# Performance work log

Hardware: AMD Instinct MI355X
Metric: run time of the kernel (lower is better)

Reference implementation:

```python
import jax, jax.numpy as jnp
import numpy as np

H = 768      # hidden_size
NH = 12      # num_heads
HD = H // NH # head_dim = 64


def setup_inputs() -> dict:
    key = jax.random.key(0)
    k1, k2, k3 = jax.random.split(key, 3)
    x = jax.random.normal(k1, (4, 2048, H), dtype=jnp.float32)
    # nn.Linear weights are [out, in]; we store transposed [in, out] for x @ W
    w_qkv = jax.random.normal(k2, (H, 3 * H), dtype=jnp.float32) * (1.0 / np.sqrt(H))
    w_out = jax.random.normal(k3, (H, H), dtype=jnp.float32) * (1.0 / np.sqrt(H))
    return {"x": x, "w_qkv": w_qkv, "w_out": w_out}


def reference(x, w_qkv, w_out):
    B, S, _ = x.shape
    qkv = (x @ w_qkv).reshape(B, S, 3, NH, HD)
    qkv = jnp.transpose(qkv, (2, 0, 3, 1, 4))  # [3, B, NH, S, HD]
    q, k, v = qkv[0], qkv[1], qkv[2]
    scale = 1.0 / np.sqrt(HD)
    scores = jnp.einsum('bhqd,bhkd->bhqk', q, k) * scale  # [B,NH,S,S]
    causal = jnp.tril(jnp.ones((S, S), dtype=bool))
    scores = jnp.where(causal, scores, jnp.finfo(scores.dtype).min)
    attn = jax.nn.softmax(scores, axis=-1)
    out = jnp.einsum('bhqk,bhkd->bhqd', attn, v)          # [B,NH,S,HD]
    out = jnp.transpose(out, (0, 2, 1, 3)).reshape(B, S, H)
    return out @ w_out
```

## Files before the change

kernel.cpp:

```cpp
#include <hip/hip_runtime.h>
#include <type_traits>

#define S_LEN 2048
#define HID   768
#define NHEAD 12
#define HDIM  64
#define BATCH 4

typedef __attribute__((ext_vector_type(4))) float float4v;
typedef __attribute__((ext_vector_type(8))) short short8;
typedef __attribute__((ext_vector_type(4))) short short4v;
typedef __attribute__((ext_vector_type(2))) int int2v;

__device__ __forceinline__ short f2b(float f) {
  unsigned u = __float_as_uint(f);
  u += 0x7fff + ((u >> 16) & 1);
  return (short)(u >> 16);
}

__device__ __forceinline__ unsigned pkbf(float a, float b) {
#if __has_builtin(__builtin_amdgcn_cvt_pk_bf16_f32)
  typedef __attribute__((ext_vector_type(2))) __bf16 bf2;
  bf2 r = __builtin_amdgcn_cvt_pk_bf16_f32(a, b);
  return *(unsigned*)&r;
#else
  return ((unsigned)(unsigned short)f2b(a)) |
         (((unsigned)(unsigned short)f2b(b)) << 16);
#endif
}

__device__ __forceinline__ float fexp2(float x) {
#if __has_builtin(__builtin_amdgcn_exp2f)
  return __builtin_amdgcn_exp2f(x);
#else
  return __expf(x * 0.69314718056f);
#endif
}

__device__ __forceinline__ void g2l16(const short* g, short* l) {
  __builtin_amdgcn_global_load_lds(
      (const __attribute__((address_space(1))) void*)g,
      (__attribute__((address_space(3))) void*)l, 16, 0, 0);
}

__global__ __launch_bounds__(256) void prepass(const float* __restrict__ x,
                                               const float* __restrict__ w_qkv,
                                               const float* __restrict__ w_out,
                                               short* __restrict__ xb,
                                               short* __restrict__ wqkvT,
                                               short* __restrict__ woutT) {
  __shared__ float tile[64][65];
  const int blk = blockIdx.x;
  if (blk < 3072) {
    int i = blk * 2048 + threadIdx.x * 8;
    float4v a = *(const float4v*)&x[i];
    float4v b = *(const float4v*)&x[i + 4];
    short8 o;
#pragma unroll
    for (int j = 0; j < 4; j++) { o[j] = f2b(a[j]); o[j + 4] = f2b(b[j]); }
    *(short8*)&xb[i] = o;
    return;
  }
  const float* W; short* WT; int N_, scaleN, idx;
  if (blk < 3504) { idx = blk - 3072; W = w_qkv; WT = wqkvT; N_ = 3 * HID; scaleN = HID; }
  else            { idx = blk - 3504; W = w_out; WT = woutT; N_ = HID;     scaleN = 0;  }
  const int nblk = N_ / 64;
  const int n0 = (idx % nblk) * 64, k0 = (idx / nblk) * 64;
  const int tx = threadIdx.x & 63, ty = threadIdx.x >> 6;
#pragma unroll
  for (int r = 0; r < 16; r++) {
    int row = r * 4 + ty;
    tile[row][tx] = W[(size_t)(k0 + row) * N_ + n0 + tx];
  }
  __syncthreads();
#pragma unroll
  for (int r = 0; r < 16; r++) {
    int row = r * 4 + ty;
    float sc = (n0 + row < scaleN) ? 0.18033688011f : 1.0f;
    WT[(size_t)(n0 + row) * HID + k0 + tx] = f2b(tile[tx][row] * sc);
  }
}

template <int OUT>
__global__ __launch_bounds__(256) void gemm_bt(const short* __restrict__ A,
                                               const short* __restrict__ Bt,
                                               float* __restrict__ Cf,
                                               short* __restrict__ Cq,
                                               short* __restrict__ vT,
                                               int M, int N, int K) {
  __shared__ __align__(16) short As[2][128 * 32];
  __shared__ __align__(16) short Bs[2][128 * 32];
  const int tid = threadIdx.x;
  const int w = tid >> 6, lane = tid & 63;
  const int quad = lane >> 4, lm = lane & 15;
  const int m0 = blockIdx.y * 128, n0 = blockIdx.x * 128;
  const int mo = (w & 1) * 64, no = (w >> 1) * 64;

  float4v acc[4][4];
#pragma unroll
  for (int i = 0; i < 4; i++)
#pragma unroll
    for (int j = 0; j < 4; j++) acc[i][j] = (float4v)0.0f;

  const int srow = w * 32 + (lane >> 2);
  const int scol = (lane & 3) * 8;
  const short* Ag = A + (size_t)(m0 + srow) * K + scol;
  const short* Bg = Bt + (size_t)(n0 + srow) * K + scol;

  for (int kb = 0; kb < K; kb += 64) {
#pragma unroll
    for (int s = 0; s < 2; s++) {
      short* Al = &As[s][(w * 32) * 32];
      short* Bl = &Bs[s][(w * 32) * 32];
      g2l16(Ag + kb + s * 32, Al);
      g2l16(Ag + kb + s * 32 + (size_t)16 * K, Al + 16 * 32);
      g2l16(Bg + kb + s * 32, Bl);
      g2l16(Bg + kb + s * 32 + (size_t)16 * K, Bl + 16 * 32);
    }
    __syncthreads();

#pragma unroll
    for (int s = 0; s < 2; s++) {
      short8 af[4], bf[4];
#pragma unroll
      for (int i = 0; i < 4; i++)
        af[i] = *(const short8*)&As[s][(mo + i * 16 + lm) * 32 + quad * 8];
#pragma unroll
      for (int j = 0; j < 4; j++)
        bf[j] = *(const short8*)&Bs[s][(no + j * 16 + lm) * 32 + quad * 8];
#pragma unroll
      for (int i = 0; i < 4; i++)
#pragma unroll
        for (int j = 0; j < 4; j++)
          acc[i][j] = __builtin_amdgcn_mfma_f32_16x16x32_bf16(af[i], bf[j], acc[i][j], 0, 0, 0);
    }
    __syncthreads();
  }

  if constexpr (OUT == 0) {
#pragma unroll
    for (int i = 0; i < 4; i++)
#pragma unroll
      for (int j = 0; j < 4; j++)
#pragma unroll
        for (int r = 0; r < 4; r++)
          Cf[(size_t)(m0 + mo + i * 16 + quad * 4 + r) * N + n0 + no + j * 16 + lm] =
              acc[i][j][r];
  } else {
    if (n0 >= 2 * HID) {
      const int b = m0 >> 11;
      const int s0 = (m0 & 2047) + mo + quad * 4;
#pragma unroll
      for (int i = 0; i < 4; i++)
#pragma unroll
        for (int j = 0; j < 4; j++) {
          int col = n0 + no + j * 16 + lm - 2 * HID;
          int h = col >> 6, d = col & 63;
          short4v pv;
#pragma unroll
          for (int r = 0; r < 4; r++) pv[r] = f2b(acc[i][j][r]);
          *(short4v*)&vT[((size_t)(b * NHEAD + h) * HDIM + d) * S_LEN + s0 + i * 16] = pv;
        }
    } else {
#pragma unroll
      for (int i = 0; i < 4; i++)
#pragma unroll
        for (int j = 0; j < 4; j++)
#pragma unroll
          for (int r = 0; r < 4; r++)
            Cq[(size_t)(m0 + mo + i * 16 + quad * 4 + r) * (2 * HID) + n0 + no + j * 16 + lm] =
                f2b(acc[i][j][r]);
    }
  }
}

__global__ __launch_bounds__(256) void attn_mfma(const short* __restrict__ qk,
                                                 const short* __restrict__ vT,
                                                 short* __restrict__ attnout) {
  __shared__ __align__(16) short Ks[2][64 * 64];
  __shared__ __align__(16) short Vt[2][64 * 64];
  __shared__ __align__(16) short Ps[4][16 * 64];

  const int tid = threadIdx.x;
  const int w = tid >> 6, lane = tid & 63;
  const int quad = lane >> 4, lm = lane & 15;
  const int bh = blockIdx.x, a = blockIdx.y;
  const int b = bh / NHEAD, h = bh % NHEAD;
  const int qtile[2] = {a, 31 - a};

  short8 aq[2][2];
#pragma unroll
  for (int t = 0; t < 2; t++)
#pragma unroll
    for (int kb = 0; kb < 2; kb++)
      aq[t][kb] = *(const short8*)&qk[(size_t)(b * S_LEN + qtile[t] * 64 + w * 16 + lm) * (2 * HID) +
                                      h * HDIM + kb * 32 + quad * 8];

  const size_t kbase = (size_t)(b * S_LEN) * (2 * HID) + HID + h * HDIM;
  const size_t vbase = (size_t)(b * NHEAD + h) * HDIM * S_LEN;
  const short* ksrc[2];
  const short* vsrc[2];
#pragma unroll
  for (int i = 0; i < 2; i++) {
    int c = (w * 2 + i) * 64 + lane;
    int row = c >> 3, slot = c & 7;
    int q8 = slot ^ (row & 7);
    int key = 4 * (row & 15) + (row >> 4);
    ksrc[i] = qk + kbase + (size_t)key * (2 * HID) + q8 * 8;
    vsrc[i] = vT + vbase + (size_t)row * S_LEN + q8 * 8;
  }

#define ISSUE(KT, BUF)                                                              \
  {                                                                                 \
    _Pragma("unroll") for (int i = 0; i < 2; i++) {                                 \
      g2l16(ksrc[i] + (size_t)(KT) * 64 * (2 * HID), &Ks[BUF][(w * 2 + i) * 512]);  \
      g2l16(vsrc[i] + (KT) * 64, &Vt[BUF][(w * 2 + i) * 512]);                      \
    }                                                                               \
  }

  float4v o_acc[2][4];
#pragma unroll
  for (int t = 0; t < 2; t++)
#pragma unroll
    for (int nt = 0; nt < 4; nt++) o_acc[t][nt] = (float4v)0.0f;
  float lsum[2][4];
#pragma unroll
  for (int t = 0; t < 2; t++)
#pragma unroll
    for (int r = 0; r < 4; r++) lsum[t][r] = 0.0f;

  const int ktmax = 32 - a;
  const int swx = (lm & 7) << 4;
  int cur = 0;

  ISSUE(0, 0);

  for (int kt = 0; kt < ktmax; kt++) {
    asm volatile("s_waitcnt vmcnt(0)" ::: "memory");
    __syncthreads();
    if (kt + 1 < ktmax) ISSUE(kt + 1, cur ^ 1);

#pragma unroll
    for (int t = 0; t < 2; t++) {
      if (t == 0 && kt > a) continue;
      float4v s_acc[4];
#pragma unroll
      for (int i = 0; i < 4; i++) s_acc[i] = (float4v)0.0f;
#pragma unroll
      for (int kb = 0; kb < 2; kb++) {
#pragma unroll
        for (int nt = 0; nt < 4; nt++) {
          short8 bk = *(const short8*)((const char*)&Ks[cur][0] +
                        ((nt * 16 + lm) << 7) + (((kb * 64 + quad * 16)) ^ swx));
          s_acc[nt] = __builtin_amdgcn_mfma_f32_16x16x32_bf16(aq[t][kb], bk, s_acc[nt], 0, 0, 0);
        }
      }

      const bool diag = (kt == qtile[t]);
#pragma unroll
      for (int r = 0; r < 4; r++) {
        float e[4];
#pragma unroll
        for (int nt = 0; nt < 4; nt++) {
          float v = fexp2(s_acc[nt][r]);
          if (diag && (4 * lm + nt > w * 16 + quad * 4 + r)) v = 0.0f;
          lsum[t][r] += v;
          e[nt] = v;
        }
        int2v p2 = {(int)pkbf(e[0], e[1]), (int)pkbf(e[2], e[3])};
        int rowp = quad * 4 + r;
        *(int2v*)((char*)&Ps[w][0] + (rowp << 7) + ((lm * 8) ^ ((rowp & 7) << 4))) = p2;
      }

#pragma unroll
      for (int kb = 0; kb < 2; kb++) {
        short8 ap = *(const short8*)((const char*)&Ps[w][0] +
                      (lm << 7) + ((kb * 64 + quad * 16) ^ swx));
#pragma unroll
        for (int nt = 0; nt < 4; nt++) {
          short8 bv = *(const short8*)((const char*)&Vt[cur][0] +
                        ((nt * 16 + lm) << 7) + ((kb * 64 + quad * 16) ^ swx));
          o_acc[t][nt] = __builtin_amdgcn_mfma_f32_16x16x32_bf16(ap, bv, o_acc[t][nt], 0, 0, 0);
        }
      }
    }
    cur ^= 1;
  }

#pragma unroll
  for (int t = 0; t < 2; t++)
#pragma unroll
    for (int r = 0; r < 4; r++) {
#pragma unroll
      for (int off = 1; off < 16; off <<= 1)
        lsum[t][r] += __shfl_xor(lsum[t][r], off, 16);
      float inv = 1.0f / lsum[t][r];
      int rowg = b * S_LEN + qtile[t] * 64 + w * 16 + quad * 4 + r;
#pragma unroll
      for (int nt = 0; nt < 4; nt++)
        attnout[(size_t)rowg * HID + h * HDIM + nt * 16 + lm] =
            f2b(o_acc[t][nt][r] * inv);
    }
#undef ISSUE
}

extern "C" void kernel_launch(void* const* d_in, const int* in_sizes, int n_in,
                              void* d_out, int out_size, void* d_ws, size_t ws_size,
                              hipStream_t stream) {
  const float* x     = (const float*)d_in[0];
  const float* w_qkv = (const float*)d_in[1];
  const float* w_out = (const float*)d_in[2];
  float* out = (float*)d_out;

  const int M = BATCH * S_LEN;
  short* qk     = (short*)d_ws;
  short* attn   = qk + (size_t)M * 2 * HID;
  short* vT     = attn + (size_t)M * HID;
  short* xb     = vT + (size_t)M * HID;
  short* wqkvT  = xb + (size_t)M * HID;
  short* woutT  = wqkvT + (size_t)(3 * HID) * HID;

  prepass<<<3648, 256, 0, stream>>>(x, w_qkv, w_out, xb, wqkvT, woutT);

  gemm_bt<1><<<dim3(3 * HID / 128, M / 128), 256, 0, stream>>>(
      xb, wqkvT, nullptr, qk, vT, M, 3 * HID, HID);
  attn_mfma<<<dim3(BATCH * NHEAD, S_LEN / 128), 256, 0, stream>>>(qk, vT, attn);
  gemm_bt<0><<<dim3(HID / 128, M / 128), 256, 0, stream>>>(
      attn, woutT, out, nullptr, nullptr, M, HID, HID);
}
```

Before: 200.6 us.

## Compute softmax row sums via MFMA with ones, remap GEMM tiles, precompute LDS addresses

The attention kernel drops the per-element scalar row-sum accumulation and the final cross-lane shuffle reduction. It instead computes row sums with an extra MFMA of the bf16 probability tile against a ones vector. LDS read/write addresses and global load pointers are precomputed and incremented rather than recomputed each iteration, and s_setprio raises wave priority around MFMA bursts. The GEMM block index is also remapped across 8 groups to change scheduling locality; the sums now come from bf16-rounded probabilities, which slightly changes numerics.

```diff
diff --git a/kernel.cpp b/kernel.cpp
--- a/kernel.cpp
+++ b/kernel.cpp
@@ -93,7 +93,12 @@
   const int tid = threadIdx.x;
   const int w = tid >> 6, lane = tid & 63;
   const int quad = lane >> 4, lm = lane & 15;
-  const int m0 = blockIdx.y * 128, n0 = blockIdx.x * 128;
+
+  const int gx = gridDim.x;
+  const int nwg = gx * gridDim.y;
+  int flat = blockIdx.y * gx + blockIdx.x;
+  if ((nwg & 7) == 0) flat = (flat & 7) * (nwg >> 3) + (flat >> 3);
+  const int m0 = (flat / gx) * 128, n0 = (flat % gx) * 128;
   const int mo = (w & 1) * 64, no = (w >> 1) * 64;
 
   float4v acc[4][4];
@@ -196,26 +201,49 @@
       aq[t][kb] = *(const short8*)&qk[(size_t)(b * S_LEN + qtile[t] * 64 + w * 16 + lm) * (2 * HID) +
                                       h * HDIM + kb * 32 + quad * 8];
 
+  const float4v z4 = (float4v)0.0f;
+  short8 one8;
+#pragma unroll
+  for (int j = 0; j < 8; j++) one8[j] = (short)0x3F80;
+
   const size_t kbase = (size_t)(b * S_LEN) * (2 * HID) + HID + h * HDIM;
   const size_t vbase = (size_t)(b * NHEAD + h) * HDIM * S_LEN;
-  const short* ksrc[2];
-  const short* vsrc[2];
+  const short* kptr[2];
+  const short* vptr[2];
 #pragma unroll
   for (int i = 0; i < 2; i++) {
     int c = (w * 2 + i) * 64 + lane;
     int row = c >> 3, slot = c & 7;
     int q8 = slot ^ (row & 7);
     int key = 4 * (row & 15) + (row >> 4);
-    ksrc[i] = qk + kbase + (size_t)key * (2 * HID) + q8 * 8;
-    vsrc[i] = vT + vbase + (size_t)row * S_LEN + q8 * 8;
-  }
-
-#define ISSUE(KT, BUF)                                                              \
-  {                                                                                 \
-    _Pragma("unroll") for (int i = 0; i < 2; i++) {                                 \
-      g2l16(ksrc[i] + (size_t)(KT) * 64 * (2 * HID), &Ks[BUF][(w * 2 + i) * 512]);  \
-      g2l16(vsrc[i] + (KT) * 64, &Vt[BUF][(w * 2 + i) * 512]);                      \
-    }                                                                               \
+    kptr[i] = qk + kbase + (size_t)key * (2 * HID) + q8 * 8;
+    vptr[i] = vT + vbase + (size_t)row * S_LEN + q8 * 8;
+  }
+
+#define ISSUE(BUF)                                                    \
+  {                                                                   \
+    _Pragma("unroll") for (int i = 0; i < 2; i++) {                   \
+      g2l16(kptr[i], &Ks[BUF][(w * 2 + i) * 512]);                    \
+      g2l16(vptr[i], &Vt[BUF][(w * 2 + i) * 512]);                    \
+      kptr[i] += 64 * 2 * HID;                                        \
+      vptr[i] += 64;                                                  \
+    }                                                                 \
+  }
+
+  const int swx = (lm & 7) << 4;
+  const int loff0 = (quad * 16) ^ swx;
+  const int loff1 = (64 + quad * 16) ^ swx;
+  const int rowK = lm << 7;
+  const char* KsB = (const char*)&Ks[0][0];
+  const char* VtB = (const char*)&Vt[0][0];
+  const char* PsW = (const char*)&Ps[w][0];
+  const char* pread0 = PsW + rowK + loff0;
+  const char* pread1 = PsW + rowK + loff1;
+  char* pswa[4];
+#pragma unroll
+  for (int r = 0; r < 4; r++) {
+    int rowp = quad * 4 + r;
+    pswa[r] = (char*)PsW + (rowp << 7) + ((lm * 8) ^ ((rowp & 7) << 4));
   }
 
   float4v o_acc[2][4];
@@ -223,38 +251,42 @@
   for (int t = 0; t < 2; t++)
 #pragma unroll
     for (int nt = 0; nt < 4; nt++) o_acc[t][nt] = (float4v)0.0f;
-  float lsum[2][4];
-#pragma unroll
-  for (int t = 0; t < 2; t++)
-#pragma unroll
-    for (int r = 0; r < 4; r++) lsum[t][r] = 0.0f;
+  float4v o1[2];
+  o1[0] = (float4v)0.0f;
+  o1[1] = (float4v)0.0f;
 
   const int ktmax = 32 - a;
-  const int swx = (lm & 7) << 4;
   int cur = 0;
 
-  ISSUE(0, 0);
+  ISSUE(0);
 
   for (int kt = 0; kt < ktmax; kt++) {
     asm volatile("s_waitcnt vmcnt(0)" ::: "memory");
     __syncthreads();
-    if (kt + 1 < ktmax) ISSUE(kt + 1, cur ^ 1);
+    if (kt + 1 < ktmax) ISSUE(cur ^ 1);
+
+    const int coff = cur << 13;
+    const char* kB0 = KsB + coff + rowK + loff0;
+    const char* kB1 = KsB + coff + rowK + loff1;
+    const char* vB0 = VtB + coff + rowK + loff0;
+    const char* vB1 = VtB + coff + rowK + loff1;
 
 #pragma unroll
     for (int t = 0; t < 2; t++) {
       if (t == 0 && kt > a) continue;
       float4v s_acc[4];
-#pragma unroll
-      for (int i = 0; i < 4; i++) s_acc[i] = (float4v)0.0f;
-#pragma unroll
-      for (int kb = 0; kb < 2; kb++) {
-#pragma unroll
-        for (int nt = 0; nt < 4; nt++) {
-          short8 bk = *(const short8*)((const char*)&Ks[cur][0] +
-                        ((nt * 16 + lm) << 7) + (((kb * 64 + quad * 16)) ^ swx));
-          s_acc[nt] = __builtin_amdgcn_mfma_f32_16x16x32_bf16(aq[t][kb], bk, s_acc[nt], 0, 0, 0);
-        }
+      __builtin_amdgcn_s_setprio(1);
+#pragma unroll
+      for (int nt = 0; nt < 4; nt++) {
+        short8 bk = *(const short8*)(kB0 + nt * 2048);
+        s_acc[nt] = __builtin_amdgcn_mfma_f32_16x16x32_bf16(aq[t][0], bk, z4, 0, 0, 0);
       }
+#pragma unroll
+      for (int nt = 0; nt < 4; nt++) {
+        short8 bk = *(const short8*)(kB1 + nt * 2048);
+        s_acc[nt] = __builtin_amdgcn_mfma_f32_16x16x32_bf16(aq[t][1], bk, s_acc[nt], 0, 0, 0);
+      }
+      __builtin_amdgcn_s_setprio(0);
 
       const bool diag = (kt == qtile[t]);
 #pragma unroll
@@ -264,25 +296,25 @@
         for (int nt = 0; nt < 4; nt++) {
           float v = fexp2(s_acc[nt][r]);
           if (diag && (4 * lm + nt > w * 16 + quad * 4 + r)) v = 0.0f;
-          lsum[t][r] += v;
           e[nt] = v;
         }
         int2v p2 = {(int)pkbf(e[0], e[1]), (int)pkbf(e[2], e[3])};
-        int rowp = quad * 4 + r;
-        *(int2v*)((char*)&Ps[w][0] + (rowp << 7) + ((lm * 8) ^ ((rowp & 7) << 4))) = p2;
+        *(int2v*)pswa[r] = p2;
       }
 
+      __builtin_amdgcn_s_setprio(1);
 #pragma unroll
       for (int kb = 0; kb < 2; kb++) {
-        short8 ap = *(const short8*)((const char*)&Ps[w][0] +
-                      (lm << 7) + ((kb * 64 + quad * 16) ^ swx));
+        short8 ap = *(const short8*)(kb ? pread1 : pread0);
+        const char* vB = kb ? vB1 : vB0;
+        o1[t] = __builtin_amdgcn_mfma_f32_16x16x32_bf16(ap, one8, o1[t], 0, 0, 0);
 #pragma unroll
         for (int nt = 0; nt < 4; nt++) {
-          short8 bv = *(const short8*)((const char*)&Vt[cur][0] +
-                        ((nt * 16 + lm) << 7) + ((kb * 64 + quad * 16) ^ swx));
+          short8 bv = *(const short8*)(vB + nt * 2048);
           o_acc[t][nt] = __builtin_amdgcn_mfma_f32_16x16x32_bf16(ap, bv, o_acc[t][nt], 0, 0, 0);
         }
       }
+      __builtin_amdgcn_s_setprio(0);
     }
     cur ^= 1;
   }
@@ -291,10 +323,7 @@
   for (int t = 0; t < 2; t++)
 #pragma unroll
     for (int r = 0; r < 4; r++) {
-#pragma unroll
-      for (int off = 1; off < 16; off <<= 1)
-        lsum[t][r] += __shfl_xor(lsum[t][r], off, 16);
-      float inv = 1.0f / lsum[t][r];
+      float inv = 1.0f / o1[t][r];
       int rowg = b * S_LEN + qtile[t] * 64 + w * 16 + quad * 4 + r;
 #pragma unroll
       for (int nt = 0; nt < 4; nt++)
```

Result: faster. 193.6 us (-3.5%).
